# Optimization experiments

Measured on AMD Instinct MI355X. Metric: run time of the kernel, lower is better.

## Reference

```python
import jax, jax.numpy as jnp
import numpy as np

B, DIM, H, W = 32, 256, 64, 64
KEY_DIM, HEADS, MAX_SHAPE = 8, 2, 64
NHKD = KEY_DIM * HEADS  # 16
SCALE = KEY_DIM ** -0.5


def setup_inputs() -> dict:
    key = jax.random.key(0)
    ks = jax.random.split(key, 20)
    rn = lambda k, s, sc=0.02: jax.random.normal(k, s, jnp.float32) * sc
    bn_s = lambda k, c: 1.0 + rn(k, (c,))
    bn_b = lambda k, c: rn(k, (c,))
    return {
        "x": jax.random.normal(ks[0], (B, DIM, H, W), jnp.float32),
        "w_qkv": rn(ks[1], (3 * NHKD, DIM), 0.05),
        "qkv_scale": bn_s(ks[2], 3 * NHKD), "qkv_shift": bn_b(ks[3], 3 * NHKD),
        "pos_h": rn(ks[4], (1, NHKD, MAX_SHAPE)),
        "pos_w": rn(ks[5], (1, NHKD, MAX_SHAPE)),
        "w_fusion": rn(ks[6], (DIM, 2 * NHKD), 0.05),
        "fusion_scale": bn_s(ks[7], DIM), "fusion_shift": bn_b(ks[8], DIM),
        "w_g1": rn(ks[9], (DIM // 4, DIM), 0.05),
        "g1_scale": bn_s(ks[10], DIM // 4), "g1_shift": bn_b(ks[11], DIM // 4),
        "w_g2": rn(ks[12], (DIM, DIM // 4), 0.05),
        "g2_scale": bn_s(ks[13], DIM), "g2_shift": bn_b(ks[14], DIM),
    }


def _interp_linear(p, out_size):
    # torch F.interpolate(mode='linear', align_corners=False) on (1,C,L)
    L = p.shape[-1]
    coords = (jnp.arange(out_size, dtype=jnp.float32) + 0.5) * (L / out_size) - 0.5
    coords = jnp.clip(coords, 0.0, L - 1)
    lo = jnp.floor(coords).astype(jnp.int32)
    hi = jnp.minimum(lo + 1, L - 1)
    w = (coords - lo).astype(p.dtype)
    return p[..., lo] * (1.0 - w) + p[..., hi] * w


def _cbn(x, w, s, b):
    # 1x1 conv (no bias) + eval-mode BN folded into per-channel scale/shift
    y = jnp.einsum('oc,bchw->bohw', w, x)
    return y * s[None, :, None, None] + b[None, :, None, None]


def _axial(q, k, v, pos):
    # q,k,v: (B, NHKD, L); pos: (1, NHKD, L)
    Bq, _, L = q.shape
    q = (q + pos).reshape(Bq, HEADS, KEY_DIM, L)
    k = (k + pos).reshape(Bq, HEADS, KEY_DIM, L)
    v = v.reshape(Bq, HEADS, KEY_DIM, L)
    attn = jax.nn.softmax(jnp.einsum('bhdi,bhdj->bhij', q, k) * SCALE, axis=-1)
    out = jnp.einsum('bhij,bhdj->bhdi', attn, v)  # (B,h,kd,L)
    return out.reshape(Bq, NHKD, L)


def _forward(x, w_qkv, qkv_scale, qkv_shift, pos_h, pos_w, w_fusion,
             fusion_scale, fusion_shift, w_g1, g1_scale, g1_shift,
             w_g2, g2_scale, g2_shift):
    Bx, C, Hx, Wx = x.shape
    qkv = _cbn(x, w_qkv, qkv_scale, qkv_shift)  # (B,3*NHKD,H,W)
    q, k, v = jnp.split(qkv, 3, axis=1)
    # height axis: mean over W
    ph = _interp_linear(pos_h, Hx)
    out_h = _axial(q.mean(-1), k.mean(-1), v.mean(-1), ph)  # (B,NHKD,H)
    # width axis: mean over H
    pw = _interp_linear(pos_w, Wx)
    out_w = _axial(q.mean(-2), k.mean(-2), v.mean(-2), pw)  # (B,NHKD,W)
    fused = jnp.concatenate([
        jnp.broadcast_to(out_h[..., None], (Bx, NHKD, Hx, Wx)),
        jnp.broadcast_to(out_w[:, :, None, :], (Bx, NHKD, Hx, Wx)),
    ], axis=1)
    output = _cbn(fused, w_fusion, fusion_scale, fusion_shift)  # (B,C,H,W)
    # SE-style detection gate
    g = output.mean(axis=(2, 3), keepdims=True)  # (B,C,1,1)
    g = jax.nn.silu(_cbn(g, w_g1, g1_scale, g1_shift))
    g = jax.nn.sigmoid(_cbn(g, w_g2, g2_scale, g2_shift))
    return x + (output * g) * 0.1


def reference(x, w_qkv, qkv_scale, qkv_shift, pos_h, pos_w, w_fusion,
              fusion_scale, fusion_shift, w_g1, g1_scale, g1_shift,
              w_g2, g2_scale, g2_shift):
    return _forward(x, w_qkv, qkv_scale, qkv_shift, pos_h, pos_w, w_fusion,
                    fusion_scale, fusion_shift, w_g1, g1_scale, g1_shift,
                    w_g2, g2_scale, g2_shift)
```

## Files before the change

kernel.cpp:

```cpp
#include <hip/hip_runtime.h>
#include <math.h>

#define NB 32
#define DIM 256
#define LHW 64
#define SCALE_QK 0.35355339059327373f

__global__ __launch_bounds__(256) void k_reduce(const float* __restrict__ x,
                                                float* __restrict__ xh,
                                                float* __restrict__ xw) {
    __shared__ float s[64 * 68];
    const int t = threadIdx.x;
    const float* p = x + (size_t)blockIdx.x * 4096;
#pragma unroll
    for (int i = 0; i < 4; ++i) {
        int idx4 = t + 256 * i;
        float4 v = reinterpret_cast<const float4*>(p)[idx4];
        int h = idx4 >> 4;
        int w0 = (idx4 & 15) << 2;
        *reinterpret_cast<float4*>(&s[h * 68 + w0]) = v;
    }
    __syncthreads();
    if (t < 64) {
        float acc = 0.f;
#pragma unroll
        for (int j = 0; j < 16; ++j) {
            float4 v = *reinterpret_cast<const float4*>(&s[t * 68 + j * 4]);
            acc += v.x + v.y + v.z + v.w;
        }
        xh[(size_t)blockIdx.x * 64 + t] = acc * (1.0f / 64.0f);
    } else if (t < 128) {
        int w = t - 64;
        float acc = 0.f;
#pragma unroll
        for (int h = 0; h < 64; ++h) acc += s[h * 68 + w];
        xw[(size_t)blockIdx.x * 64 + w] = acc * (1.0f / 64.0f);
    }
}

__global__ __launch_bounds__(256) void k_qkv_attn(
    const float* __restrict__ xh, const float* __restrict__ xw,
    const float* __restrict__ w_qkv, const float* __restrict__ qscale,
    const float* __restrict__ qshift, const float* __restrict__ pos_h,
    const float* __restrict__ pos_w, float* __restrict__ outa) {
    const int blk = blockIdx.x;
    const int head = blk & 1;
    const int axis = (blk >> 1) & 1;
    const int b = blk >> 2;
    const float* xa = (axis ? xw : xh) + (size_t)b * DIM * 64;
    const float* pos = axis ? pos_w : pos_h;

    __shared__ float smem[16384];
    float* sx = smem;
    float* sq = smem;
    float* sP = smem + 24 * 64;

    const int t = threadIdx.x;
#pragma unroll
    for (int i = 0; i < 16; ++i) {
        int idx4 = t + 256 * i;
        reinterpret_cast<float4*>(sx)[idx4] =
            reinterpret_cast<const float4*>(xa)[idx4];
    }
    __syncthreads();

    const int l = t & 63, g = t >> 6;
    float acc[6] = {0.f, 0.f, 0.f, 0.f, 0.f, 0.f};
    int ocg[6];
#pragma unroll
    for (int i = 0; i < 6; ++i) {
        int r = g + 4 * i;
        ocg[i] = (r >> 3) * 16 + head * 8 + (r & 7);
    }
    for (int c = 0; c < 256; c += 4) {
        float x0 = sx[(c + 0) * 64 + l];
        float x1 = sx[(c + 1) * 64 + l];
        float x2 = sx[(c + 2) * 64 + l];
        float x3 = sx[(c + 3) * 64 + l];
#pragma unroll
        for (int i = 0; i < 6; ++i) {
            float4 wv = *reinterpret_cast<const float4*>(&w_qkv[ocg[i] * 256 + c]);
            acc[i] += wv.x * x0 + wv.y * x1 + wv.z * x2 + wv.w * x3;
        }
    }
    __syncthreads();
    float vals[6];
#pragma unroll
    for (int i = 0; i < 6; ++i) {
        int r = g + 4 * i;
        float v = acc[i] * qscale[ocg[i]] + qshift[ocg[i]];
        if (r < 16) v += pos[(head * 8 + (r & 7)) * 64 + l];
        vals[i] = v;
    }
#pragma unroll
    for (int i = 0; i < 6; ++i) sq[(g + 4 * i) * 64 + l] = vals[i];
    __syncthreads();

    {
        const int j = t & 63;
#pragma unroll
        for (int ii = 0; ii < 16; ++ii) {
            int i = g + 4 * ii;
            float s = 0.f;
#pragma unroll
            for (int d = 0; d < 8; ++d)
                s += sq[d * 64 + i] * sq[(8 + d) * 64 + j];
            sP[i * 65 + j] = s * SCALE_QK;
        }
    }
    __syncthreads();
    if (t < 64) {
        float m = -1e30f;
        for (int j = 0; j < 64; ++j) m = fmaxf(m, sP[t * 65 + j]);
        float sum = 0.f;
        for (int j = 0; j < 64; ++j) {
            float e = __expf(sP[t * 65 + j] - m);
            sP[t * 65 + j] = e;
            sum += e;
        }
        float r = 1.0f / sum;
        for (int j = 0; j < 64; ++j) sP[t * 65 + j] *= r;
    }
    __syncthreads();
    {
        const int i = t & 63;
#pragma unroll
        for (int k2 = 0; k2 < 2; ++k2) {
            int d = g * 2 + k2;
            float acc2 = 0.f;
            for (int j = 0; j < 64; ++j)
                acc2 += sP[i * 65 + j] * sq[(16 + d) * 64 + j];
            outa[(((size_t)b * 2 + axis) * 16 + head * 8 + d) * 64 + i] = acc2;
        }
    }
}

__global__ __launch_bounds__(256) void k_fusion(
    const float* __restrict__ outa, const float* __restrict__ w_fusion,
    const float* __restrict__ fscale, const float* __restrict__ fshift,
    float* __restrict__ Ah, float* __restrict__ Aw, float* __restrict__ Amean) {
    const int blk = blockIdx.x;
    const int axis = blk & 1;
    const int b = blk >> 1;
    __shared__ float so[16 * 64];
    __shared__ float swf[256 * 16];
    const int t = threadIdx.x;
    reinterpret_cast<float4*>(so)[t] =
        reinterpret_cast<const float4*>(outa + (size_t)blk * 16 * 64)[t];
#pragma unroll
    for (int i = 0; i < 4; ++i) {
        int idx4 = t + 256 * i;
        int o = idx4 >> 2, qd = idx4 & 3;
        reinterpret_cast<float4*>(swf)[idx4] =
            *reinterpret_cast<const float4*>(&w_fusion[o * 32 + axis * 16 + qd * 4]);
    }
    __syncthreads();
    const int l = t & 63, g = t >> 6;
    float xo[16];
#pragma unroll
    for (int cc = 0; cc < 16; ++cc) xo[cc] = so[cc * 64 + l];
    float* A = (axis ? Aw : Ah) + (size_t)b * DIM * 64;
    for (int i = 0; i < 64; ++i) {
        int o = g + 4 * i;
        float acc = 0.f;
#pragma unroll
        for (int q4 = 0; q4 < 4; ++q4) {
            float4 wv = *reinterpret_cast<const float4*>(&swf[o * 16 + q4 * 4]);
            acc += wv.x * xo[q4 * 4] + wv.y * xo[q4 * 4 + 1] +
                   wv.z * xo[q4 * 4 + 2] + wv.w * xo[q4 * 4 + 3];
        }
        float val = acc * fscale[o] + (axis ? fshift[o] : 0.0f);
        A[o * 64 + l] = val;
        float s = val;
#pragma unroll
        for (int off = 32; off >= 1; off >>= 1) s += __shfl_xor(s, off, 64);
        if (l == 0) Amean[(size_t)blk * DIM + o] = s * (1.0f / 64.0f);
    }
}

__global__ __launch_bounds__(256) void k_gate(
    const float* __restrict__ Amean, const float* __restrict__ w_g1,
    const float* __restrict__ g1s, const float* __restrict__ g1b,
    const float* __restrict__ w_g2, const float* __restrict__ g2s,
    const float* __restrict__ g2b, float* __restrict__ g2out) {
    const int b = blockIdx.x;
    __shared__ float sg[256];
    __shared__ float sg1[64];
    const int t = threadIdx.x;
    sg[t] = Amean[(size_t)(b * 2) * 256 + t] + Amean[(size_t)(b * 2 + 1) * 256 + t];
    __syncthreads();
    if (t < 64) {
        float acc = 0.f;
        for (int c = 0; c < 256; c += 4) {
            float4 wv = *reinterpret_cast<const float4*>(&w_g1[t * 256 + c]);
            acc += wv.x * sg[c] + wv.y * sg[c + 1] + wv.z * sg[c + 2] + wv.w * sg[c + 3];
        }
        float v = acc * g1s[t] + g1b[t];
        sg1[t] = v / (1.0f + __expf(-v));
    }
    __syncthreads();
    {
        float acc = 0.f;
        for (int j = 0; j < 64; j += 4) {
            float4 wv = *reinterpret_cast<const float4*>(&w_g2[t * 64 + j]);
            acc += wv.x * sg1[j] + wv.y * sg1[j + 1] + wv.z * sg1[j + 2] + wv.w * sg1[j + 3];
        }
        float v = acc * g2s[t] + g2b[t];
        g2out[(size_t)b * 256 + t] = 0.1f / (1.0f + __expf(-v));
    }
}

__global__ __launch_bounds__(256) void k_final(
    const float* __restrict__ x, const float* __restrict__ Ah,
    const float* __restrict__ Aw, const float* __restrict__ g2,
    float* __restrict__ out) {
    const int bo = blockIdx.x;
    __shared__ float sAh[64], sAw[64];
    const int t = threadIdx.x;
    if (t < 64) sAh[t] = Ah[(size_t)bo * 64 + t];
    else if (t < 128) sAw[t - 64] = Aw[(size_t)bo * 64 + (t - 64)];
    const float gv = g2[bo];
    __syncthreads();
    const float* px = x + (size_t)bo * 4096;
    float* po = out + (size_t)bo * 4096;
#pragma unroll
    for (int i = 0; i < 4; ++i) {
        int idx4 = t + 256 * i;
        float4 xv = reinterpret_cast<const float4*>(px)[idx4];
        int h = idx4 >> 4, w0 = (idx4 & 15) << 2;
        float a = sAh[h];
        float4 r;
        r.x = xv.x + gv * (a + sAw[w0 + 0]);
        r.y = xv.y + gv * (a + sAw[w0 + 1]);
        r.z = xv.z + gv * (a + sAw[w0 + 2]);
        r.w = xv.w + gv * (a + sAw[w0 + 3]);
        reinterpret_cast<float4*>(po)[idx4] = r;
    }
}

extern "C" void kernel_launch(void* const* d_in, const int* in_sizes, int n_in,
                              void* d_out, int out_size, void* d_ws, size_t ws_size,
                              hipStream_t stream) {
    const float* x      = (const float*)d_in[0];
    const float* w_qkv  = (const float*)d_in[1];
    const float* qscale = (const float*)d_in[2];
    const float* qshift = (const float*)d_in[3];
    const float* pos_h  = (const float*)d_in[4];
    const float* pos_w  = (const float*)d_in[5];
    const float* w_fus  = (const float*)d_in[6];
    const float* fscale = (const float*)d_in[7];
    const float* fshift = (const float*)d_in[8];
    const float* w_g1   = (const float*)d_in[9];
    const float* g1s    = (const float*)d_in[10];
    const float* g1b    = (const float*)d_in[11];
    const float* w_g2   = (const float*)d_in[12];
    const float* g2s    = (const float*)d_in[13];
    const float* g2b    = (const float*)d_in[14];
    float* out = (float*)d_out;

    float* ws    = (float*)d_ws;
    float* xh    = ws;
    float* xw    = xh + 524288;
    float* outa  = xw + 524288;
    float* Ah    = outa + 65536;
    float* Aw    = Ah + 524288;
    float* Amean = Aw + 524288;
    float* g2w   = Amean + 16384;

    k_reduce<<<NB * DIM, 256, 0, stream>>>(x, xh, xw);
    k_qkv_attn<<<NB * 4, 256, 0, stream>>>(xh, xw, w_qkv, qscale, qshift,
                                           pos_h, pos_w, outa);
    k_fusion<<<NB * 2, 256, 0, stream>>>(outa, w_fus, fscale, fshift, Ah, Aw, Amean);
    k_gate<<<NB, 256, 0, stream>>>(Amean, w_g1, g1s, g1b, w_g2, g2s, g2b, g2w);
    k_final<<<NB * DIM, 256, 0, stream>>>(x, Ah, Aw, g2w, out);
}
```

Before: 328.6 us.

## Drop fusion kernel; compute gate from attention means and fuse projection into final

Removes the separate fusion kernel that materialised the full per-channel Ah/Aw maps. The gate input is now derived from per-channel means of the attention outputs, pushed through the linear fusion projection. The final kernel recomputes the 16-channel projection per output channel from the attention outputs and writes with nontemporal stores. This removes one launch and several MB of intermediate traffic, in exchange for redundant small projection work in every final block.

Measured after the change: 307.8 us. 1.07x faster.

```diff
diff --git a/kernel.cpp b/kernel.cpp
--- a/kernel.cpp
+++ b/kernel.cpp
@@ -3,8 +3,9 @@
 
 #define NB 32
 #define DIM 256
-#define LHW 64
 #define SCALE_QK 0.35355339059327373f
+
+typedef float floatx4 __attribute__((ext_vector_type(4)));
 
 __global__ __launch_bounds__(256) void k_reduce(const float* __restrict__ x,
                                                 float* __restrict__ xh,
@@ -42,7 +43,8 @@
     const float* __restrict__ xh, const float* __restrict__ xw,
     const float* __restrict__ w_qkv, const float* __restrict__ qscale,
     const float* __restrict__ qshift, const float* __restrict__ pos_h,
-    const float* __restrict__ pos_w, float* __restrict__ outa) {
+    const float* __restrict__ pos_w, float* __restrict__ outa,
+    float* __restrict__ outam) {
     const int blk = blockIdx.x;
     const int head = blk & 1;
     const int axis = (blk >> 1) & 1;
@@ -131,63 +133,38 @@
             for (int j = 0; j < 64; ++j)
                 acc2 += sP[i * 65 + j] * sq[(16 + d) * 64 + j];
             outa[(((size_t)b * 2 + axis) * 16 + head * 8 + d) * 64 + i] = acc2;
-        }
-    }
-}
-
-__global__ __launch_bounds__(256) void k_fusion(
-    const float* __restrict__ outa, const float* __restrict__ w_fusion,
+            float s = acc2;
+#pragma unroll
+            for (int off = 32; off >= 1; off >>= 1) s += __shfl_xor(s, off, 64);
+            if (i == 0)
+                outam[((size_t)b * 2 + axis) * 16 + head * 8 + d] = s * (1.0f / 64.0f);
+        }
+    }
+}
+
+__global__ __launch_bounds__(256) void k_gate(
+    const float* __restrict__ outam, const float* __restrict__ w_fusion,
     const float* __restrict__ fscale, const float* __restrict__ fshift,
-    float* __restrict__ Ah, float* __restrict__ Aw, float* __restrict__ Amean) {
-    const int blk = blockIdx.x;
-    const int axis = blk & 1;
-    const int b = blk >> 1;
-    __shared__ float so[16 * 64];
-    __shared__ float swf[256 * 16];
-    const int t = threadIdx.x;
-    reinterpret_cast<float4*>(so)[t] =
-        reinterpret_cast<const float4*>(outa + (size_t)blk * 16 * 64)[t];
-#pragma unroll
-    for (int i = 0; i < 4; ++i) {
-        int idx4 = t + 256 * i;
-        int o = idx4 >> 2, qd = idx4 & 3;
-        reinterpret_cast<float4*>(swf)[idx4] =
-            *reinterpret_cast<const float4*>(&w_fusion[o * 32 + axis * 16 + qd * 4]);
-    }
-    __syncthreads();
-    const int l = t & 63, g = t >> 6;
-    float xo[16];
-#pragma unroll
-    for (int cc = 0; cc < 16; ++cc) xo[cc] = so[cc * 64 + l];
-    float* A = (axis ? Aw : Ah) + (size_t)b * DIM * 64;
-    for (int i = 0; i < 64; ++i) {
-        int o = g + 4 * i;
-        float acc = 0.f;
-#pragma unroll
-        for (int q4 = 0; q4 < 4; ++q4) {
-            float4 wv = *reinterpret_cast<const float4*>(&swf[o * 16 + q4 * 4]);
-            acc += wv.x * xo[q4 * 4] + wv.y * xo[q4 * 4 + 1] +
-                   wv.z * xo[q4 * 4 + 2] + wv.w * xo[q4 * 4 + 3];
-        }
-        float val = acc * fscale[o] + (axis ? fshift[o] : 0.0f);
-        A[o * 64 + l] = val;
-        float s = val;
-#pragma unroll
-        for (int off = 32; off >= 1; off >>= 1) s += __shfl_xor(s, off, 64);
-        if (l == 0) Amean[(size_t)blk * DIM + o] = s * (1.0f / 64.0f);
-    }
-}
-
-__global__ __launch_bounds__(256) void k_gate(
-    const float* __restrict__ Amean, const float* __restrict__ w_g1,
-    const float* __restrict__ g1s, const float* __restrict__ g1b,
-    const float* __restrict__ w_g2, const float* __restrict__ g2s,
-    const float* __restrict__ g2b, float* __restrict__ g2out) {
+    const float* __restrict__ w_g1, const float* __restrict__ g1s,
+    const float* __restrict__ g1b, const float* __restrict__ w_g2,
+    const float* __restrict__ g2s, const float* __restrict__ g2b,
+    float* __restrict__ g2out) {
     const int b = blockIdx.x;
+    __shared__ float sm[32];
     __shared__ float sg[256];
     __shared__ float sg1[64];
     const int t = threadIdx.x;
-    sg[t] = Amean[(size_t)(b * 2) * 256 + t] + Amean[(size_t)(b * 2 + 1) * 256 + t];
+    if (t < 32) sm[t] = outam[(size_t)b * 32 + t];
+    __syncthreads();
+    {
+        float acc = 0.f;
+#pragma unroll
+        for (int c = 0; c < 32; c += 4) {
+            float4 wv = *reinterpret_cast<const float4*>(&w_fusion[t * 32 + c]);
+            acc += wv.x * sm[c] + wv.y * sm[c + 1] + wv.z * sm[c + 2] + wv.w * sm[c + 3];
+        }
+        sg[t] = acc * fscale[t] + fshift[t];
+    }
     __syncthreads();
     if (t < 64) {
         float acc = 0.f;
@@ -201,6 +178,7 @@
     __syncthreads();
     {
         float acc = 0.f;
+#pragma unroll
         for (int j = 0; j < 64; j += 4) {
             float4 wv = *reinterpret_cast<const float4*>(&w_g2[t * 64 + j]);
             acc += wv.x * sg1[j] + wv.y * sg1[j + 1] + wv.z * sg1[j + 2] + wv.w * sg1[j + 3];
@@ -211,15 +189,33 @@
 }
 
 __global__ __launch_bounds__(256) void k_final(
-    const float* __restrict__ x, const float* __restrict__ Ah,
-    const float* __restrict__ Aw, const float* __restrict__ g2,
+    const float* __restrict__ x, const float* __restrict__ outa,
+    const float* __restrict__ w_fusion, const float* __restrict__ fscale,
+    const float* __restrict__ fshift, const float* __restrict__ g2,
     float* __restrict__ out) {
     const int bo = blockIdx.x;
-    __shared__ float sAh[64], sAw[64];
-    const int t = threadIdx.x;
-    if (t < 64) sAh[t] = Ah[(size_t)bo * 64 + t];
-    else if (t < 128) sAw[t - 64] = Aw[(size_t)bo * 64 + (t - 64)];
+    const int b = bo >> 8, o = bo & 255;
+    __shared__ float so[2048];
+    __shared__ float sP[64], sQ[64];
+    const int t = threadIdx.x;
+    const float* oa = outa + (size_t)b * 2048;
+    reinterpret_cast<float4*>(so)[t] = reinterpret_cast<const float4*>(oa)[t];
+    reinterpret_cast<float4*>(so)[t + 256] = reinterpret_cast<const float4*>(oa)[t + 256];
     const float gv = g2[bo];
+    __syncthreads();
+    if (t < 64) {
+        float acc = 0.f;
+#pragma unroll
+        for (int c = 0; c < 16; ++c) acc += w_fusion[o * 32 + c] * so[c * 64 + t];
+        sP[t] = gv * (fscale[o] * acc + fshift[o]);
+    } else if (t < 128) {
+        int w = t - 64;
+        float acc = 0.f;
+#pragma unroll
+        for (int c = 0; c < 16; ++c)
+            acc += w_fusion[o * 32 + 16 + c] * so[1024 + c * 64 + w];
+        sQ[w] = gv * fscale[o] * acc;
+    }
     __syncthreads();
     const float* px = x + (size_t)bo * 4096;
     float* po = out + (size_t)bo * 4096;
@@ -228,13 +224,13 @@
         int idx4 = t + 256 * i;
         float4 xv = reinterpret_cast<const float4*>(px)[idx4];
         int h = idx4 >> 4, w0 = (idx4 & 15) << 2;
-        float a = sAh[h];
-        float4 r;
-        r.x = xv.x + gv * (a + sAw[w0 + 0]);
-        r.y = xv.y + gv * (a + sAw[w0 + 1]);
-        r.z = xv.z + gv * (a + sAw[w0 + 2]);
-        r.w = xv.w + gv * (a + sAw[w0 + 3]);
-        reinterpret_cast<float4*>(po)[idx4] = r;
+        float a = sP[h];
+        floatx4 r;
+        r.x = xv.x + a + sQ[w0 + 0];
+        r.y = xv.y + a + sQ[w0 + 1];
+        r.z = xv.z + a + sQ[w0 + 2];
+        r.w = xv.w + a + sQ[w0 + 3];
+        __builtin_nontemporal_store(r, reinterpret_cast<floatx4*>(po) + idx4);
     }
 }
 
@@ -262,15 +258,13 @@
     float* xh    = ws;
     float* xw    = xh + 524288;
     float* outa  = xw + 524288;
-    float* Ah    = outa + 65536;
-    float* Aw    = Ah + 524288;
-    float* Amean = Aw + 524288;
-    float* g2w   = Amean + 16384;
+    float* outam = outa + 65536;
+    float* g2w   = outam + 1024;
 
     k_reduce<<<NB * DIM, 256, 0, stream>>>(x, xh, xw);
     k_qkv_attn<<<NB * 4, 256, 0, stream>>>(xh, xw, w_qkv, qscale, qshift,
-                                           pos_h, pos_w, outa);
-    k_fusion<<<NB * 2, 256, 0, stream>>>(outa, w_fus, fscale, fshift, Ah, Aw, Amean);
-    k_gate<<<NB, 256, 0, stream>>>(Amean, w_g1, g1s, g1b, w_g2, g2s, g2b, g2w);
-    k_final<<<NB * DIM, 256, 0, stream>>>(x, Ah, Aw, g2w, out);
-}
+                                           pos_h, pos_w, outa, outam);
+    k_gate<<<NB, 256, 0, stream>>>(outam, w_fus, fscale, fshift,
+                                   w_g1, g1s, g1b, w_g2, g2s, g2b, g2w);
+    k_final<<<NB * DIM, 256, 0, stream>>>(x, outa, w_fus, fscale, fshift, g2w, out);
+}
```
